# Optimization experiments

Measured on AMD Instinct MI355X. Metric: run time of the kernel, lower is better.

The kernel has to match this reference:

```python
import jax, jax.numpy as jnp
import numpy as np

B, G, D, H, L, FFN = 4, 2048, 256, 8, 4, 1024
HD = D // H
BASE = 100.0
MASK_ID = -10.0
LN_EPS = 1e-5


def setup_inputs() -> dict:
    key = jax.random.key(0)
    ks = jax.random.split(key, 18)
    s = 0.02
    f32 = jnp.float32
    return {
        "x": jax.random.uniform(ks[0], (B, G), f32, 0.0, 8.0),
        "gene_emb": jax.random.normal(ks[1], (G, D), f32) * s,
        "Wq": jax.random.normal(ks[2], (L, D, D), f32) * s,
        "bq": jnp.zeros((L, D), f32),
        "Wk": jax.random.normal(ks[3], (L, D, D), f32) * s,
        "bk": jnp.zeros((L, D), f32),
        "Wv": jax.random.normal(ks[4], (L, D, D), f32) * s,
        "bv": jnp.zeros((L, D), f32),
        "ln1_g": jnp.ones((L, D), f32),
        "ln1_b": jnp.zeros((L, D), f32),
        "ln2_g": jnp.ones((L, D), f32),
        "ln2_b": jnp.zeros((L, D), f32),
        "WU": jax.random.normal(ks[5], (L, D, FFN), f32) * s,
        "bU": jnp.zeros((L, FFN), f32),
        "WV": jax.random.normal(ks[6], (L, FFN, D), f32) * s,
        "bV": jnp.zeros((L, D), f32),
        "Wo": jax.random.normal(ks[7], (D, 1), f32) * s,
        "bo": jnp.zeros((1,), f32),
    }


def _ln(x, g, b):
    mu = jnp.mean(x, axis=-1, keepdims=True)
    var = jnp.mean(jnp.square(x - mu), axis=-1, keepdims=True)
    return (x - mu) * jax.lax.rsqrt(var + LN_EPS) * g + b


def _linear_attn(z, Wq, bq, Wk, bk, Wv, bv):
    # feature_type='sqr': phi(u) = u**2; causal (compute_type='iter') linear attention
    q = jnp.square(z @ Wq + bq).reshape(B, G, H, HD)
    k = jnp.square(z @ Wk + bk).reshape(B, G, H, HD)
    v = (z @ Wv + bv).reshape(B, G, H, HD)
    kv = jnp.cumsum(jnp.einsum('bshm,bshd->bshmd', k, v), axis=1)  # prefix sums of k (x) v
    ksum = jnp.cumsum(k, axis=1)
    num = jnp.einsum('bshm,bshmd->bshd', q, kv)
    den = jnp.einsum('bshm,bshm->bsh', q, ksum)
    return (num / (den[..., None] + 1e-16)).reshape(B, G, D)


def reference(x, gene_emb, Wq, bq, Wk, bk, Wv, bv, ln1_g, ln1_b, ln2_g, ln2_b,
              WU, bU, WV, bV, Wo, bo):
    # rotary expression embedding
    inv_freq = 1.0 / BASE ** (jnp.arange(0, D, 2, dtype=jnp.float32) / D)  # [D/2]
    freqs = x[:, :, None] * inv_freq                                       # [B,G,D/2]
    ree = jnp.concatenate([jnp.sin(freqs), jnp.cos(freqs)], axis=-1)       # [B,G,D]
    ree = jnp.where((x == MASK_ID)[..., None], 0.0, ree)
    h = gene_emb[None] + ree
    for l in range(L):
        # pre-LN attention block
        h = h + _linear_attn(_ln(h, ln1_g[l], ln1_b[l]), Wq[l], bq[l], Wk[l], bk[l], Wv[l], bv[l])
        # pre-LN FFN block (exact erf gelu, as torch F.gelu default)
        z = _ln(h, ln2_g[l], ln2_b[l])
        h = h + jax.nn.gelu(z @ WU[l] + bU[l], approximate=False) @ WV[l] + bV[l]
    return (h @ Wo + bo)[..., 0]  # [B,G]
```

## Files before the change

### kernel.cpp

```cpp
#include <hip/hip_runtime.h>
#include <math.h>

constexpr int kB = 4, kG = 2048, kD = 256, kH = 8, kHD = 32, kL = 4, kFFN = 1024;
constexpr int kBG = kB * kG;
constexpr int kCHUNK = 64;
constexpr int kNC = kG / kCHUNK;
constexpr int kSUMSZ = kHD * kHD + kHD;
constexpr int kQKVN = 3 * kD;

typedef __bf16 bf16x8 __attribute__((ext_vector_type(8)));
typedef unsigned short ushort8 __attribute__((ext_vector_type(8)));
typedef float floatx4 __attribute__((ext_vector_type(4)));

__device__ __forceinline__ unsigned short f2bf(float f) {
  unsigned int u = __float_as_uint(f);
  u += 0x7fff + ((u >> 16) & 1);
  return (unsigned short)(u >> 16);
}

__device__ __forceinline__ void load_lds_16(const void* g, void* l) {
  __builtin_amdgcn_global_load_lds((const __attribute__((address_space(1))) void*)g,
                                   (__attribute__((address_space(3))) void*)l,
                                   16, 0, 0);
}

__global__ void embed_kernel(const float* __restrict__ x,
                             const float* __restrict__ ge,
                             float* __restrict__ h) {
  int idx = blockIdx.x * 256 + threadIdx.x;
  int d = idx & (kD - 1);
  int g = (idx >> 8) & (kG - 1);
  int b = idx >> 19;
  float xv = x[b * kG + g];
  int i = d & 127;
  float inv = expf(-(float)i * (4.6051701859880914f / 128.0f));
  float f = xv * inv;
  float r = (d < 128) ? sinf(f) : cosf(f);
  if (xv == -10.0f) r = 0.0f;
  h[idx] = ge[g * kD + d] + r;
}

__global__ void convert_weights_kernel(
    const float* __restrict__ Wq, const float* __restrict__ Wk,
    const float* __restrict__ Wv, const float* __restrict__ WU,
    const float* __restrict__ WV, const float* __restrict__ bq,
    const float* __restrict__ bk, const float* __restrict__ bv,
    unsigned short* __restrict__ Wqkv_t, unsigned short* __restrict__ WU_t,
    unsigned short* __restrict__ WV_t, float* __restrict__ bias_qkv) {
  int blk = blockIdx.x;
  if (blk >= kL * 704) {
    int idx = (blk - kL * 704) * 256 + threadIdx.x;
    if (idx < kL * kQKVN) {
      int l = idx / kQKVN, n = idx % kQKVN;
      float v = (n < 256) ? bq[l * 256 + n]
              : (n < 512) ? bk[l * 256 + n - 256]
                          : bv[l * 256 + n - 512];
      bias_qkv[idx] = v;
    }
    return;
  }
  int l = blk / 704, id = blk % 704;
  const float* src;
  unsigned short* dst;
  int Ksrc, Nsrc, kt, nt;
  if (id < 192) {
    int m = id >> 6, tid = id & 63;
    src = (m == 0 ? Wq : m == 1 ? Wk : Wv) + (size_t)l * 256 * 256;
    dst = Wqkv_t + (size_t)l * kQKVN * 256 + (size_t)m * 256 * 256;
    Ksrc = 256; Nsrc = 256; kt = tid >> 3; nt = tid & 7;
  } else if (id < 448) {
    int tid = id - 192;
    src = WU + (size_t)l * 256 * 1024;
    dst = WU_t + (size_t)l * 1024 * 256;
    Ksrc = 256; Nsrc = 1024; kt = tid >> 5; nt = tid & 31;
  } else {
    int tid = id - 448;
    src = WV + (size_t)l * 1024 * 256;
    dst = WV_t + (size_t)l * 256 * 1024;
    Ksrc = 1024; Nsrc = 256; kt = tid >> 3; nt = tid & 7;
  }
  __shared__ float s[32][33];
  int tx = threadIdx.x & 31, ty = threadIdx.x >> 5;
#pragma unroll
  for (int r = 0; r < 4; r++)
    s[ty + r * 8][tx] = src[(size_t)(kt * 32 + ty + r * 8) * Nsrc + nt * 32 + tx];
  __syncthreads();
#pragma unroll
  for (int r = 0; r < 4; r++)
    dst[(size_t)(nt * 32 + ty + r * 8) * Ksrc + kt * 32 + tx] =
        f2bf(s[tx][ty + r * 8]);
}

__global__ __launch_bounds__(256) void ln_kernel(
    const float* __restrict__ h, const float* __restrict__ gamma,
    const float* __restrict__ beta, unsigned short* __restrict__ z) {
  int w = threadIdx.x >> 6, lane = threadIdx.x & 63;
  size_t row = (size_t)blockIdx.x * 4 + w;
  float4 v = *(const float4*)&h[row * kD + lane * 4];
  float s = v.x + v.y + v.z + v.w;
  float sq = v.x * v.x + v.y * v.y + v.z * v.z + v.w * v.w;
#pragma unroll
  for (int o = 32; o > 0; o >>= 1) {
    s += __shfl_xor(s, o);
    sq += __shfl_xor(sq, o);
  }
  float mu = s * (1.0f / kD);
  float var = sq * (1.0f / kD) - mu * mu;
  float r = rsqrtf(var + 1e-5f);
  float4 g4 = *(const float4*)&gamma[lane * 4];
  float4 b4 = *(const float4*)&beta[lane * 4];
  float y0 = (v.x - mu) * r * g4.x + b4.x;
  float y1 = (v.y - mu) * r * g4.y + b4.y;
  float y2 = (v.z - mu) * r * g4.z + b4.z;
  float y3 = (v.w - mu) * r * g4.w + b4.w;
  unsigned int u0 = (unsigned int)f2bf(y0) | ((unsigned int)f2bf(y1) << 16);
  unsigned int u1 = (unsigned int)f2bf(y2) | ((unsigned int)f2bf(y3) << 16);
  uint2 uu; uu.x = u0; uu.y = u1;
  *(uint2*)&z[row * kD + lane * 4] = uu;
}

template <int EPI>
__global__ __launch_bounds__(256) void mfma_gemm(
    const unsigned short* __restrict__ A, const unsigned short* __restrict__ Bt,
    const float* __restrict__ bias, void* __restrict__ Cout,
    const float* __restrict__ Cres, int M, int N, int K) {
  __shared__ unsigned short As[64 * 32];
  __shared__ unsigned short Bs[64 * 32];
  const int t = threadIdx.x;
  const int w = t >> 6, lane = t & 63;
  const int bm = blockIdx.y * 64, bn = blockIdx.x * 64;
  const int wm = (w >> 1) * 32, wn = (w & 1) * 32;

  const int srow = lane >> 2;
  const int skof = (lane & 3) * 8;
  const unsigned short* ap = A + (size_t)(bm + w * 16 + srow) * K + skof;
  const unsigned short* bp = Bt + (size_t)(bn + w * 16 + srow) * K + skof;
  unsigned short* asd = &As[w * 512];
  unsigned short* bsd = &Bs[w * 512];

  floatx4 acc[2][2];
#pragma unroll
  for (int i = 0; i < 2; i++)
#pragma unroll
    for (int j = 0; j < 2; j++) acc[i][j] = (floatx4){0.f, 0.f, 0.f, 0.f};

  const int lm = lane & 15, lq = lane >> 4;
  const unsigned short* afp = &As[(wm + lm) * 32 + lq * 8];
  const unsigned short* bfp = &Bs[(wn + lm) * 32 + lq * 8];

  for (int k0 = 0; k0 < K; k0 += 32) {
    load_lds_16(ap + k0, asd);
    load_lds_16(bp + k0, bsd);
    __syncthreads();
    bf16x8 af[2], bfr[2];
#pragma unroll
    for (int i = 0; i < 2; i++)
      af[i] = __builtin_bit_cast(bf16x8,
          *reinterpret_cast<const ushort8*>(afp + i * 16 * 32));
#pragma unroll
    for (int j = 0; j < 2; j++)
      bfr[j] = __builtin_bit_cast(bf16x8,
          *reinterpret_cast<const ushort8*>(bfp + j * 16 * 32));
#pragma unroll
    for (int i = 0; i < 2; i++)
#pragma unroll
      for (int j = 0; j < 2; j++)
        acc[i][j] = __builtin_amdgcn_mfma_f32_16x16x32_bf16(af[i], bfr[j],
                                                            acc[i][j], 0, 0, 0);
    __syncthreads();
  }

  const int r0 = bm + wm + lq * 4;
  const int c0 = bn + wn + lm;
#pragma unroll
  for (int j = 0; j < 2; j++) {
    int col = c0 + j * 16;
    float bv = bias[col];
#pragma unroll
    for (int i = 0; i < 2; i++) {
      int rowb = r0 + i * 16;
#pragma unroll
      for (int r = 0; r < 4; r++) {
        int row = rowb + r;
        float v = acc[i][j][r] + bv;
        size_t idx = (size_t)row * N + col;
        if (EPI == 1) {
          ((float*)Cout)[idx] = (col < 512) ? v * v : v;
        } else if (EPI == 2) {
          float g = 0.5f * v * (1.0f + erff(v * 0.70710678118654752f));
          ((unsigned short*)Cout)[idx] = f2bf(g);
        } else {
          ((float*)Cout)[idx] = Cres[idx] + v;
        }
      }
    }
  }
}

__global__ __launch_bounds__(256) void attn_sums_kernel(
    const float* __restrict__ qkv, float* __restrict__ sums) {
  int blk = blockIdx.x;
  int c = blk & (kNC - 1);
  int hh = (blk >> 5) & (kH - 1);
  int b = blk >> 8;
  int g0 = c * kCHUNK;
  __shared__ float ks[kCHUNK][kHD];
  __shared__ float vs[kCHUNK][kHD];
  const float* kbase = qkv + (size_t)(b * kG + g0) * kQKVN + 256 + hh * kHD;
  const float* vbase = qkv + (size_t)(b * kG + g0) * kQKVN + 512 + hh * kHD;
#pragma unroll
  for (int r = 0; r < 2; r++) {
    int e = threadIdx.x + r * 256;
    int i = e >> 3, j = (e & 7) * 4;
    *(float4*)&ks[i][j] = *(const float4*)&kbase[(size_t)i * kQKVN + j];
    *(float4*)&vs[i][j] = *(const float4*)&vbase[(size_t)i * kQKVN + j];
  }
  __syncthreads();
  int m = threadIdx.x >> 3, n0 = (threadIdx.x & 7) * 4;
  float a0 = 0, a1 = 0, a2 = 0, a3 = 0;
  for (int i = 0; i < kCHUNK; i++) {
    float km = ks[i][m];
    float4 v4 = *(const float4*)&vs[i][n0];
    a0 = fmaf(km, v4.x, a0); a1 = fmaf(km, v4.y, a1);
    a2 = fmaf(km, v4.z, a2); a3 = fmaf(km, v4.w, a3);
  }
  float* outp = sums + (size_t)blk * kSUMSZ;
  *(float4*)&outp[m * kHD + n0] = make_float4(a0, a1, a2, a3);
  if (threadIdx.x < kHD) {
    float s = 0;
    for (int i = 0; i < kCHUNK; i++) s += ks[i][threadIdx.x];
    outp[kHD * kHD + threadIdx.x] = s;
  }
}

__global__ void attn_scan_kernel(float* __restrict__ sums) {
  int bh = blockIdx.x / 5, part = blockIdx.x % 5;
  int e = part * 256 + threadIdx.x;
  if (e >= kSUMSZ) return;
  float* base = sums + (size_t)bh * kNC * kSUMSZ + e;
  float v[kNC];
#pragma unroll
  for (int c = 0; c < kNC; c++) v[c] = base[(size_t)c * kSUMSZ];
  float run = 0;
#pragma unroll
  for (int c = 0; c < kNC; c++) {
    float tv = v[c];
    base[(size_t)c * kSUMSZ] = run;
    run += tv;
  }
}

__global__ __launch_bounds__(256) void attn_out_kernel(
    const float* __restrict__ qkv, const float* __restrict__ sums,
    float* __restrict__ h) {
  int blk = blockIdx.x;
  int c = blk & (kNC - 1);
  int hh = (blk >> 5) & (kH - 1);
  int b = blk >> 8;
  int g0 = c * kCHUNK;
  __shared__ float qs[kCHUNK][36];
  __shared__ float ks[kCHUNK][36];
  __shared__ float vs[kCHUNK][36];
  __shared__ float Sf[kHD][kHD];
  __shared__ float ksum[kHD];
  __shared__ float dinv_s[kCHUNK];
  __shared__ float Amat[kCHUNK][68];
  int t = threadIdx.x;
  const float* base = qkv + (size_t)(b * kG + g0) * kQKVN + hh * kHD;
#pragma unroll
  for (int r = 0; r < 2; r++) {
    int e = t + r * 256;
    int i = e >> 3, j = (e & 7) * 4;
    *(float4*)&qs[i][j] = *(const float4*)&base[(size_t)i * kQKVN + j];
    *(float4*)&ks[i][j] = *(const float4*)&base[(size_t)i * kQKVN + 256 + j];
    *(float4*)&vs[i][j] = *(const float4*)&base[(size_t)i * kQKVN + 512 + j];
  }
  const float* sp = sums + (size_t)blk * kSUMSZ;
  *(float4*)&((float*)Sf)[t * 4] = *(const float4*)&sp[t * 4];
  if (t < 8) *(float4*)&ksum[t * 4] = *(const float4*)&sp[kHD * kHD + t * 4];
  __syncthreads();

  {
    int i = t >> 2, jb = t & 3;
    float qr[kHD];
#pragma unroll
    for (int m4 = 0; m4 < kHD / 4; m4++) {
      float4 qv = *(const float4*)&qs[i][m4 * 4];
      qr[m4 * 4 + 0] = qv.x; qr[m4 * 4 + 1] = qv.y;
      qr[m4 * 4 + 2] = qv.z; qr[m4 * 4 + 3] = qv.w;
    }
    float psum = 0.0f;
#pragma unroll
    for (int jj = 0; jj < 16; jj++) {
      int j = jb + jj * 4;
      float s = 0;
#pragma unroll
      for (int m4 = 0; m4 < kHD / 4; m4++) {
        float4 kv = *(const float4*)&ks[j][m4 * 4];
        s = fmaf(qr[m4 * 4 + 0], kv.x, s);
        s = fmaf(qr[m4 * 4 + 1], kv.y, s);
        s = fmaf(qr[m4 * 4 + 2], kv.z, s);
        s = fmaf(qr[m4 * 4 + 3], kv.w, s);
      }
      Amat[i][j] = s;
      if (j <= i) psum += s;
    }
    psum += __shfl_xor(psum, 1);
    psum += __shfl_xor(psum, 2);
    if (jb == 0) {
      float dk = 0;
#pragma unroll
      for (int m = 0; m < kHD; m++) dk = fmaf(qr[m], ksum[m], dk);
      dinv_s[i] = 1.0f / (psum + dk + 1e-16f);
    }
  }
  __syncthreads();

  float* hbase = h + (size_t)(b * kG + g0) * kD + hh * kHD;
#pragma unroll
  for (int uu = 0; uu < 2; uu++) {
    int u = t + uu * 256;
    int i = u >> 3, n0 = (u & 7) * 4;
    float ax = 0, ay = 0, az = 0, aw = 0;
#pragma unroll
    for (int m = 0; m < kHD; m++) {
      float qm = qs[i][m];
      float4 s4 = *(const float4*)&Sf[m][n0];
      ax = fmaf(qm, s4.x, ax); ay = fmaf(qm, s4.y, ay);
      az = fmaf(qm, s4.z, az); aw = fmaf(qm, s4.w, aw);
    }
    for (int j = 0; j <= i; j++) {
      float w = Amat[i][j];
      float4 vv = *(const float4*)&vs[j][n0];
      ax = fmaf(w, vv.x, ax); ay = fmaf(w, vv.y, ay);
      az = fmaf(w, vv.z, az); aw = fmaf(w, vv.w, aw);
    }
    float dinv = dinv_s[i];
    float* hp = hbase + (size_t)i * kD + n0;
    float4 old = *(const float4*)hp;
    *(float4*)hp = make_float4(old.x + ax * dinv, old.y + ay * dinv,
                               old.z + az * dinv, old.w + aw * dinv);
  }
}

__global__ __launch_bounds__(256) void final_kernel(
    const float* __restrict__ h, const float* __restrict__ Wo,
    const float* __restrict__ bo, float* __restrict__ out) {
  int w = threadIdx.x >> 6, lane = threadIdx.x & 63;
  size_t row = (size_t)blockIdx.x * 4 + w;
  float4 hv = *(const float4*)&h[row * kD + lane * 4];
  float4 wv = *(const float4*)&Wo[lane * 4];
  float s = hv.x * wv.x + hv.y * wv.y + hv.z * wv.z + hv.w * wv.w;
#pragma unroll
  for (int o = 32; o > 0; o >>= 1) s += __shfl_xor(s, o);
  if (lane == 0) out[row] = s + bo[0];
}

extern "C" void kernel_launch(void* const* d_in, const int* in_sizes, int n_in,
                              void* d_out, int out_size, void* d_ws, size_t ws_size,
                              hipStream_t stream) {
  const float* x    = (const float*)d_in[0];
  const float* ge   = (const float*)d_in[1];
  const float* Wq   = (const float*)d_in[2];
  const float* bq   = (const float*)d_in[3];
  const float* Wk   = (const float*)d_in[4];
  const float* bk   = (const float*)d_in[5];
  const float* Wv   = (const float*)d_in[6];
  const float* bv   = (const float*)d_in[7];
  const float* ln1g = (const float*)d_in[8];
  const float* ln1b = (const float*)d_in[9];
  const float* ln2g = (const float*)d_in[10];
  const float* ln2b = (const float*)d_in[11];
  const float* WU   = (const float*)d_in[12];
  const float* bU   = (const float*)d_in[13];
  const float* WV   = (const float*)d_in[14];
  const float* bV   = (const float*)d_in[15];
  const float* Wo   = (const float*)d_in[16];
  const float* bo   = (const float*)d_in[17];
  float* out = (float*)d_out;

  float* ws = (float*)d_ws;
  float*          h       = ws;
  unsigned short* zb      = (unsigned short*)(ws + 2097152);
  float*          qkv     = ws + 3145728;
  unsigned short* u       = (unsigned short*)qkv;
  float*          sums    = ws + 9437184;
  unsigned short* Wqkv_t  = (unsigned short*)(ws + 10518528);
  unsigned short* WU_t    = (unsigned short*)(ws + 10911744);
  unsigned short* WV_t    = (unsigned short*)(ws + 11436032);
  float*          bias_qkv= ws + 11960320;

  dim3 blk256(256);
  convert_weights_kernel<<<kL * 704 + 12, blk256, 0, stream>>>(
      Wq, Wk, Wv, WU, WV, bq, bk, bv, Wqkv_t, WU_t, WV_t, bias_qkv);
  embed_kernel<<<kBG * kD / 256, blk256, 0, stream>>>(x, ge, h);
  for (int l = 0; l < kL; l++) {
    ln_kernel<<<kBG / 4, blk256, 0, stream>>>(h, ln1g + l * kD, ln1b + l * kD, zb);
    mfma_gemm<1><<<dim3(kQKVN / 64, kBG / 64), blk256, 0, stream>>>(
        zb, Wqkv_t + (size_t)l * kQKVN * kD, bias_qkv + l * kQKVN, qkv, nullptr,
        kBG, kQKVN, kD);
    attn_sums_kernel<<<kB * kH * kNC, blk256, 0, stream>>>(qkv, sums);
    attn_scan_kernel<<<kB * kH * 5, blk256, 0, stream>>>(sums);
    attn_out_kernel<<<kB * kH * kNC, blk256, 0, stream>>>(qkv, sums, h);
    ln_kernel<<<kBG / 4, blk256, 0, stream>>>(h, ln2g + l * kD, ln2b + l * kD, zb);
    mfma_gemm<2><<<dim3(kFFN / 64, kBG / 64), blk256, 0, stream>>>(
        zb, WU_t + (size_t)l * kFFN * kD, bU + l * kFFN, u, nullptr,
        kBG, kFFN, kD);
    mfma_gemm<3><<<dim3(kD / 64, kBG / 64), blk256, 0, stream>>>(
        u, WV_t + (size_t)l * kD * kFFN, bV + l * kD, h, h,
        kBG, kD, kFFN);
  }
  final_kernel<<<kBG / 4, blk256, 0, stream>>>(h, Wo, bo, out);
}
```

Measured before the change: 425.9 us.

## Fuse LayerNorm into GEMM prologue, stage full-K tiles, fold scan into attn_out

Removes the standalone LayerNorm kernels. The QKV and FFN-up GEMMs now read fp32 h directly and compute per-row statistics in the prologue, writing bf16 normalized rows into padded LDS. The GEMM stages 256-wide K slabs (eight 32-wide chunks) per barrier instead of one 32-wide chunk, which cuts synchronisation count. The separate prefix-scan kernel is dropped: each attn_out block sums the preceding chunk sums itself. That adds redundant loads for later chunks and recomputes LN across column blocks, but saves launches and round trips through global memory.

After: 931.9 us. 119% more time.

```diff
diff --git a/kernel.cpp b/kernel.cpp
--- a/kernel.cpp
+++ b/kernel.cpp
@@ -91,52 +91,22 @@
         f2bf(s[tx][ty + r * 8]);
 }
 
-__global__ __launch_bounds__(256) void ln_kernel(
-    const float* __restrict__ h, const float* __restrict__ gamma,
-    const float* __restrict__ beta, unsigned short* __restrict__ z) {
-  int w = threadIdx.x >> 6, lane = threadIdx.x & 63;
-  size_t row = (size_t)blockIdx.x * 4 + w;
-  float4 v = *(const float4*)&h[row * kD + lane * 4];
-  float s = v.x + v.y + v.z + v.w;
-  float sq = v.x * v.x + v.y * v.y + v.z * v.z + v.w * v.w;
-#pragma unroll
-  for (int o = 32; o > 0; o >>= 1) {
-    s += __shfl_xor(s, o);
-    sq += __shfl_xor(sq, o);
-  }
-  float mu = s * (1.0f / kD);
-  float var = sq * (1.0f / kD) - mu * mu;
-  float r = rsqrtf(var + 1e-5f);
-  float4 g4 = *(const float4*)&gamma[lane * 4];
-  float4 b4 = *(const float4*)&beta[lane * 4];
-  float y0 = (v.x - mu) * r * g4.x + b4.x;
-  float y1 = (v.y - mu) * r * g4.y + b4.y;
-  float y2 = (v.z - mu) * r * g4.z + b4.z;
-  float y3 = (v.w - mu) * r * g4.w + b4.w;
-  unsigned int u0 = (unsigned int)f2bf(y0) | ((unsigned int)f2bf(y1) << 16);
-  unsigned int u1 = (unsigned int)f2bf(y2) | ((unsigned int)f2bf(y3) << 16);
-  uint2 uu; uu.x = u0; uu.y = u1;
-  *(uint2*)&z[row * kD + lane * 4] = uu;
-}
-
-template <int EPI>
+template <int EPI, bool LNFUSE, int KTOT>
 __global__ __launch_bounds__(256) void mfma_gemm(
-    const unsigned short* __restrict__ A, const unsigned short* __restrict__ Bt,
-    const float* __restrict__ bias, void* __restrict__ Cout,
-    const float* __restrict__ Cres, int M, int N, int K) {
-  __shared__ unsigned short As[64 * 32];
-  __shared__ unsigned short Bs[64 * 32];
+    const unsigned short* __restrict__ A, const float* __restrict__ Af,
+    const unsigned short* __restrict__ Bt, const float* __restrict__ bias,
+    const float* __restrict__ gamma, const float* __restrict__ beta,
+    void* __restrict__ Cout, const float* __restrict__ Cres, int M, int N) {
+  constexpr int AST = LNFUSE ? 40 : 32;
+  constexpr int ACH = 64 * AST;
+  __shared__ unsigned short As[8 * ACH];
+  __shared__ unsigned short Bs[8 * 64 * 32];
   const int t = threadIdx.x;
   const int w = t >> 6, lane = t & 63;
   const int bm = blockIdx.y * 64, bn = blockIdx.x * 64;
   const int wm = (w >> 1) * 32, wn = (w & 1) * 32;
-
   const int srow = lane >> 2;
   const int skof = (lane & 3) * 8;
-  const unsigned short* ap = A + (size_t)(bm + w * 16 + srow) * K + skof;
-  const unsigned short* bp = Bt + (size_t)(bn + w * 16 + srow) * K + skof;
-  unsigned short* asd = &As[w * 512];
-  unsigned short* bsd = &Bs[w * 512];
 
   floatx4 acc[2][2];
 #pragma unroll
@@ -145,29 +115,79 @@
     for (int j = 0; j < 2; j++) acc[i][j] = (floatx4){0.f, 0.f, 0.f, 0.f};
 
   const int lm = lane & 15, lq = lane >> 4;
-  const unsigned short* afp = &As[(wm + lm) * 32 + lq * 8];
-  const unsigned short* bfp = &Bs[(wn + lm) * 32 + lq * 8];
-
-  for (int k0 = 0; k0 < K; k0 += 32) {
-    load_lds_16(ap + k0, asd);
-    load_lds_16(bp + k0, bsd);
+
+  for (int k0 = 0; k0 < KTOT; k0 += 256) {
+    if (k0) __syncthreads();
+    const unsigned short* bp =
+        Bt + (size_t)(bn + w * 16 + srow) * KTOT + k0 + skof;
+#pragma unroll
+    for (int kc = 0; kc < 8; kc++)
+      load_lds_16(bp + kc * 32, &Bs[kc * 2048 + w * 512]);
+    if (LNFUSE) {
+      int row = t >> 2, cg = t & 3;
+      const float* hp = Af + (size_t)(bm + row) * 256 + cg * 64;
+      float va[64];
+#pragma unroll
+      for (int i = 0; i < 16; i++)
+        *(float4*)&va[i * 4] = *(const float4*)&hp[i * 4];
+      float s = 0, sq = 0;
+#pragma unroll
+      for (int i = 0; i < 64; i++) { s += va[i]; sq += va[i] * va[i]; }
+      s += __shfl_xor(s, 1);  s += __shfl_xor(s, 2);
+      sq += __shfl_xor(sq, 1); sq += __shfl_xor(sq, 2);
+      float mu = s * (1.0f / kD);
+      float var = sq * (1.0f / kD) - mu * mu;
+      float rr = rsqrtf(var + 1e-5f);
+#pragma unroll
+      for (int i = 0; i < 16; i++) {
+        float4 g4 = *(const float4*)&gamma[cg * 64 + i * 4];
+        float4 b4 = *(const float4*)&beta[cg * 64 + i * 4];
+        va[i * 4 + 0] = (va[i * 4 + 0] - mu) * rr * g4.x + b4.x;
+        va[i * 4 + 1] = (va[i * 4 + 1] - mu) * rr * g4.y + b4.y;
+        va[i * 4 + 2] = (va[i * 4 + 2] - mu) * rr * g4.z + b4.z;
+        va[i * 4 + 3] = (va[i * 4 + 3] - mu) * rr * g4.w + b4.w;
+      }
+#pragma unroll
+      for (int half = 0; half < 2; half++) {
+        int chunk = cg * 2 + half;
+        unsigned short* dst = &As[chunk * ACH + row * AST];
+#pragma unroll
+        for (int gi = 0; gi < 4; gi++) {
+          ushort8 pk;
+#pragma unroll
+          for (int e = 0; e < 8; e++)
+            pk[e] = f2bf(va[half * 32 + gi * 8 + e]);
+          *(ushort8*)&dst[gi * 8] = pk;
+        }
+      }
+    } else {
+      const unsigned short* ap =
+          A + (size_t)(bm + w * 16 + srow) * KTOT + k0 + skof;
+#pragma unroll
+      for (int kc = 0; kc < 8; kc++)
+        load_lds_16(ap + kc * 32, &As[kc * ACH + w * 512]);
+    }
     __syncthreads();
-    bf16x8 af[2], bfr[2];
-#pragma unroll
-    for (int i = 0; i < 2; i++)
-      af[i] = __builtin_bit_cast(bf16x8,
-          *reinterpret_cast<const ushort8*>(afp + i * 16 * 32));
-#pragma unroll
-    for (int j = 0; j < 2; j++)
-      bfr[j] = __builtin_bit_cast(bf16x8,
-          *reinterpret_cast<const ushort8*>(bfp + j * 16 * 32));
-#pragma unroll
-    for (int i = 0; i < 2; i++)
+#pragma unroll
+    for (int kc = 0; kc < 8; kc++) {
+      const unsigned short* afp = &As[kc * ACH + (wm + lm) * AST + lq * 8];
+      const unsigned short* bfp = &Bs[kc * 2048 + (wn + lm) * 32 + lq * 8];
+      bf16x8 af[2], bfr[2];
+#pragma unroll
+      for (int i = 0; i < 2; i++)
+        af[i] = __builtin_bit_cast(bf16x8,
+            *reinterpret_cast<const ushort8*>(afp + i * 16 * AST));
 #pragma unroll
       for (int j = 0; j < 2; j++)
-        acc[i][j] = __builtin_amdgcn_mfma_f32_16x16x32_bf16(af[i], bfr[j],
-                                                            acc[i][j], 0, 0, 0);
-    __syncthreads();
+        bfr[j] = __builtin_bit_cast(bf16x8,
+            *reinterpret_cast<const ushort8*>(bfp + j * 16 * 32));
+#pragma unroll
+      for (int i = 0; i < 2; i++)
+#pragma unroll
+        for (int j = 0; j < 2; j++)
+          acc[i][j] = __builtin_amdgcn_mfma_f32_16x16x32_bf16(af[i], bfr[j],
+                                                              acc[i][j], 0, 0, 0);
+    }
   }
 
   const int r0 = bm + wm + lq * 4;
@@ -230,23 +250,6 @@
     float s = 0;
     for (int i = 0; i < kCHUNK; i++) s += ks[i][threadIdx.x];
     outp[kHD * kHD + threadIdx.x] = s;
-  }
-}
-
-__global__ void attn_scan_kernel(float* __restrict__ sums) {
-  int bh = blockIdx.x / 5, part = blockIdx.x % 5;
-  int e = part * 256 + threadIdx.x;
-  if (e >= kSUMSZ) return;
-  float* base = sums + (size_t)bh * kNC * kSUMSZ + e;
-  float v[kNC];
-#pragma unroll
-  for (int c = 0; c < kNC; c++) v[c] = base[(size_t)c * kSUMSZ];
-  float run = 0;
-#pragma unroll
-  for (int c = 0; c < kNC; c++) {
-    float tv = v[c];
-    base[(size_t)c * kSUMSZ] = run;
-    run += tv;
   }
 }
 
@@ -275,9 +278,24 @@
     *(float4*)&ks[i][j] = *(const float4*)&base[(size_t)i * kQKVN + 256 + j];
     *(float4*)&vs[i][j] = *(const float4*)&base[(size_t)i * kQKVN + 512 + j];
   }
-  const float* sp = sums + (size_t)blk * kSUMSZ;
-  *(float4*)&((float*)Sf)[t * 4] = *(const float4*)&sp[t * 4];
-  if (t < 8) *(float4*)&ksum[t * 4] = *(const float4*)&sp[kHD * kHD + t * 4];
+  {
+    float accv[5] = {0.f, 0.f, 0.f, 0.f, 0.f};
+    const float* pb = sums + (size_t)((b * kH + hh) * kNC) * kSUMSZ;
+    for (int cc = 0; cc < c; cc++) {
+      const float* pc = pb + (size_t)cc * kSUMSZ;
+#pragma unroll
+      for (int r = 0; r < 5; r++) {
+        int e = r * 256 + t;
+        if (e < kSUMSZ) accv[r] += pc[e];
+      }
+    }
+#pragma unroll
+    for (int r = 0; r < 5; r++) {
+      int e = r * 256 + t;
+      if (e < 1024) ((float*)Sf)[e] = accv[r];
+      else if (e < kSUMSZ) ksum[e - 1024] = accv[r];
+    }
+  }
   __syncthreads();
 
   {
@@ -381,7 +399,6 @@
 
   float* ws = (float*)d_ws;
   float*          h       = ws;
-  unsigned short* zb      = (unsigned short*)(ws + 2097152);
   float*          qkv     = ws + 3145728;
   unsigned short* u       = (unsigned short*)qkv;
   float*          sums    = ws + 9437184;
@@ -395,20 +412,17 @@
       Wq, Wk, Wv, WU, WV, bq, bk, bv, Wqkv_t, WU_t, WV_t, bias_qkv);
   embed_kernel<<<kBG * kD / 256, blk256, 0, stream>>>(x, ge, h);
   for (int l = 0; l < kL; l++) {
-    ln_kernel<<<kBG / 4, blk256, 0, stream>>>(h, ln1g + l * kD, ln1b + l * kD, zb);
-    mfma_gemm<1><<<dim3(kQKVN / 64, kBG / 64), blk256, 0, stream>>>(
-        zb, Wqkv_t + (size_t)l * kQKVN * kD, bias_qkv + l * kQKVN, qkv, nullptr,
-        kBG, kQKVN, kD);
+    mfma_gemm<1, true, 256><<<dim3(kQKVN / 64, kBG / 64), blk256, 0, stream>>>(
+        nullptr, h, Wqkv_t + (size_t)l * kQKVN * kD, bias_qkv + l * kQKVN,
+        ln1g + l * kD, ln1b + l * kD, qkv, nullptr, kBG, kQKVN);
     attn_sums_kernel<<<kB * kH * kNC, blk256, 0, stream>>>(qkv, sums);
-    attn_scan_kernel<<<kB * kH * 5, blk256, 0, stream>>>(sums);
     attn_out_kernel<<<kB * kH * kNC, blk256, 0, stream>>>(qkv, sums, h);
-    ln_kernel<<<kBG / 4, blk256, 0, stream>>>(h, ln2g + l * kD, ln2b + l * kD, zb);
-    mfma_gemm<2><<<dim3(kFFN / 64, kBG / 64), blk256, 0, stream>>>(
-        zb, WU_t + (size_t)l * kFFN * kD, bU + l * kFFN, u, nullptr,
-        kBG, kFFN, kD);
-    mfma_gemm<3><<<dim3(kD / 64, kBG / 64), blk256, 0, stream>>>(
-        u, WV_t + (size_t)l * kD * kFFN, bV + l * kD, h, h,
-        kBG, kD, kFFN);
+    mfma_gemm<2, true, 256><<<dim3(kFFN / 64, kBG / 64), blk256, 0, stream>>>(
+        nullptr, h, WU_t + (size_t)l * kFFN * kD, bU + l * kFFN,
+        ln2g + l * kD, ln2b + l * kD, u, nullptr, kBG, kFFN);
+    mfma_gemm<3, false, 1024><<<dim3(kD / 64, kBG / 64), blk256, 0, stream>>>(
+        u, nullptr, WV_t + (size_t)l * kD * kFFN, bV + l * kD,
+        nullptr, nullptr, h, h, kBG, kD);
   }
   final_kernel<<<kBG / 4, blk256, 0, stream>>>(h, Wo, bo, out);
 }
```
